# Kernel optimization log

Measured on AMD Instinct MI355X. Metric: run time of the kernel, lower is better.

Reference implementation:

```python
import jax, jax.numpy as jnp
import numpy as np

# Config (matches init_kwargs): 32 heads * 64 head_dim = intermediate 2048 = 2*1024
H, P, HID, N, G, K, CS = 32, 64, 1024, 128, 1, 4, 256
INTER = H * P                      # intermediate_size = expand * hidden_size
CONV_DIM = INTER + 2 * G * N       # 2304
PROJ = INTER + CONV_DIM + H        # 4384 (d_mlp == 0)
EPS = 1e-5


def segsum(x):
    """Stable segment sum: out[..., i, j] = sum_{j < k <= i} x[..., k]; -inf above diagonal."""
    T = x.shape[-1]
    xx = jnp.broadcast_to(x[..., None], x.shape + (T,))
    xx = jnp.where(jnp.tril(jnp.ones((T, T), bool), -1), xx, 0.0)
    s = jnp.cumsum(xx, axis=-2)
    return jnp.where(jnp.tril(jnp.ones((T, T), bool)), s, -jnp.inf)


def setup_inputs() -> dict:
    key = jax.random.key(0)
    ks = jax.random.split(key, 8)
    B_, S = 2, 2048
    x = jax.random.normal(ks[0], (B_, S, HID), jnp.float32)
    W_in = jax.random.normal(ks[1], (PROJ, HID), jnp.float32) / np.sqrt(HID)
    b_in = jnp.zeros((PROJ,), jnp.float32)
    conv_w = jax.random.normal(ks[2], (CONV_DIM, K), jnp.float32) / np.sqrt(K)
    # dt_bias = inverse-softplus of dt ~ LogUniform(1e-3, 0.1), as in __init__
    dt = jnp.exp(jax.random.uniform(ks[3], (H,)) * (np.log(0.1) - np.log(1e-3)) + np.log(1e-3))
    dt = jnp.clip(dt, 1e-4)
    dt_bias = dt + jnp.log(-jnp.expm1(-dt))
    A_log = jnp.log(jax.random.uniform(ks[4], (H,), minval=1.0, maxval=16.0))
    D = jnp.ones((H,), jnp.float32)
    norm_w = jnp.ones((INTER,), jnp.float32)
    W_out = jax.random.normal(ks[5], (HID, INTER), jnp.float32) / np.sqrt(INTER)
    b_out = jnp.zeros((HID,), jnp.float32)
    return {"x": x, "W_in": W_in, "b_in": b_in, "conv_w": conv_w, "dt_bias": dt_bias,
            "A_log": A_log, "D": D, "norm_w": norm_w, "W_out": W_out, "b_out": b_out}


def reference(x, W_in, b_in, conv_w, dt_bias, A_log, D, norm_w, W_out, b_out):
    B_, S, _ = x.shape
    proj = x @ W_in.T + b_in                               # (B,S,PROJ); d_mlp = 0
    gate = proj[..., :INTER]
    hBC = proj[..., INTER:INTER + CONV_DIM]
    dt = proj[..., INTER + CONV_DIM:]                      # (B,S,H)

    # depthwise causal conv1d (padding K-1, truncate to S) + silu
    xp = jnp.pad(hBC, ((0, 0), (K - 1, 0), (0, 0)))
    conv = sum(xp[:, i:i + S, :] * conv_w[:, i] for i in range(K))
    hBC = jax.nn.silu(conv)
    h = hBC[..., :INTER]
    Bm = hBC[..., INTER:INTER + G * N]
    Cm = hBC[..., INTER + G * N:]

    A = -jnp.exp(A_log.astype(jnp.float32))                # (H,)
    dt = jax.nn.softplus(dt + dt_bias)                     # (B,S,H); time_step_limit=(0,inf)
    h = h.reshape(B_, S, H, P).astype(jnp.float32)
    Bm = jnp.tile(Bm.reshape(B_, S, G, N).astype(jnp.float32), (1, 1, H // G, 1))
    Cm = jnp.tile(Cm.reshape(B_, S, G, N).astype(jnp.float32), (1, 1, H // G, 1))

    pad = (-S) % CS
    D_res = D[..., None] * jnp.pad(h, ((0, 0), (0, pad), (0, 0), (0, 0)))
    h = h * dt[..., None]
    Adt = A * dt                                           # (B,S,H)

    def chunk(t):
        t = jnp.pad(t, [(0, 0), (0, pad)] + [(0, 0)] * (t.ndim - 2))
        return t.reshape(B_, -1, CS, *t.shape[2:])

    h_c, B_c, C_c = chunk(h), chunk(Bm), chunk(Cm)         # (B,C,L,H,{P|N})
    A_c = chunk(Adt).transpose(0, 3, 1, 2)                 # (B,H,C,L)
    A_cum = jnp.cumsum(A_c, axis=-1)

    # 1) intra-chunk (diagonal blocks)
    Lmat = jnp.exp(segsum(A_c))                            # (B,H,C,L,L)
    Gm = jnp.einsum('bclhn,bcshn->bclsh', C_c, B_c)
    M = Gm * Lmat.transpose(0, 2, 3, 4, 1)
    Y_diag = jnp.einsum('bclsh,bcshp->bclhp', M, h_c)

    # 2) per-chunk final states
    decay = jnp.exp(A_cum[..., -1:] - A_cum)               # (B,H,C,L)
    B_decay = B_c * decay.transpose(0, 2, 3, 1)[..., None]
    states = jnp.einsum('bclhn,bclhp->bchpn', B_decay, h_c)

    # 3) inter-chunk state recurrence
    states = jnp.concatenate([jnp.zeros_like(states[:, :1]), states], axis=1)
    dc = jnp.exp(segsum(jnp.pad(A_cum[..., -1], ((0, 0), (0, 0), (1, 0)))))  # (B,H,C+1,C+1)
    states = jnp.einsum('bhij,bjhpn->bihpn', dc, states)[:, :-1]             # (B,C,H,P,N)

    # 4) state -> output
    sdo = jnp.exp(A_cum).transpose(0, 2, 3, 1)             # (B,C,L,H)
    Y_off = jnp.einsum('bclhn,bchpn->bclhp', C_c, states) * sdo[..., None]

    y = (Y_diag + Y_off).reshape(B_, -1, H, P) + D_res
    y = y[:, :S].reshape(B_, S, INTER)

    # gated RMSNorm (norm_before_gate=False): gate first, then normalize
    g = y * jax.nn.silu(gate.astype(jnp.float32))
    g = g * jax.lax.rsqrt(jnp.mean(g * g, axis=-1, keepdims=True) + EPS) * norm_w
    return g.astype(x.dtype) @ W_out.T + b_out
```

## Files before the change

### kernel.cpp

```cpp
#include <hip/hip_runtime.h>
#include <math.h>

#define Hh     32
#define Pp     64
#define HIDc   1024
#define Nn     128
#define CSc    256
#define INTERc 2048
#define CONVDc 2304
#define PROJc  4384
#define Bb     2
#define Ss     2048
#define Tt     4096
#define NCc    8
#define PROJ_PAD 4480

typedef __attribute__((ext_vector_type(8))) short short8_t;
typedef __attribute__((ext_vector_type(4))) float f32x4;
typedef unsigned short ushort_t;

__device__ __forceinline__ ushort_t f2b_rtn(float f) {
  unsigned u = __float_as_uint(f);
  unsigned lsb = (u >> 16) & 1u;
  u += 0x7fffu + lsb;
  return (ushort_t)(u >> 16);
}
__device__ __forceinline__ float b2f(ushort_t u) {
  return __uint_as_float(((unsigned)u) << 16);
}

__global__ __launch_bounds__(256)
void f2b_kernel(const float* __restrict__ in, ushort_t* __restrict__ out, int n8) {
  const int i = blockIdx.x * 256 + threadIdx.x;
  if (i >= n8) return;
  const float4* ip = (const float4*)in;
  float4 a = ip[2 * i], b = ip[2 * i + 1];
  union { short8_t v; ushort_t h[8]; } u;
  u.h[0] = f2b_rtn(a.x); u.h[1] = f2b_rtn(a.y);
  u.h[2] = f2b_rtn(a.z); u.h[3] = f2b_rtn(a.w);
  u.h[4] = f2b_rtn(b.x); u.h[5] = f2b_rtn(b.y);
  u.h[6] = f2b_rtn(b.z); u.h[7] = f2b_rtn(b.w);
  ((short8_t*)out)[i] = u.v;
}

__global__ __launch_bounds__(256)
void gemm_bf16(const ushort_t* __restrict__ A, const ushort_t* __restrict__ B,
               const float* __restrict__ bias, float* __restrict__ C,
               int M, int Nr, int K) {
  __shared__ ushort_t As[128 * 32];
  __shared__ ushort_t Bs[128 * 32];
  const int tid = threadIdx.x;
  const int lane = tid & 63, wid = tid >> 6;
  const int row0 = blockIdx.y * 128, col0 = blockIdx.x * 128;
  const int wr = (wid >> 1) * 64, wc = (wid & 1) * 64;
  const int fr = lane & 15;
  const int kq = (lane >> 4) * 8;

  f32x4 acc[4][4];
#pragma unroll
  for (int m = 0; m < 4; ++m)
#pragma unroll
    for (int n = 0; n < 4; ++n) acc[m][n] = (f32x4){0.f, 0.f, 0.f, 0.f};

  const int srow = (lane >> 2);
  const int skk = (lane & 3) * 8;

  for (int k0 = 0; k0 < K; k0 += 32) {
#pragma unroll
    for (int j = 0; j < 2; ++j) {
      const int s = wid * 2 + j;
      const int r = s * 16 + srow;
      const ushort_t* ga = A + (size_t)(row0 + r) * K + k0 + skk;
      const ushort_t* gb = B + (size_t)(col0 + r) * K + k0 + skk;
      __builtin_amdgcn_global_load_lds(
          (const __attribute__((address_space(1))) unsigned int*)ga,
          (__attribute__((address_space(3))) unsigned int*)(As + s * 512), 16, 0, 0);
      __builtin_amdgcn_global_load_lds(
          (const __attribute__((address_space(1))) unsigned int*)gb,
          (__attribute__((address_space(3))) unsigned int*)(Bs + s * 512), 16, 0, 0);
    }
    __syncthreads();
    short8_t av[4], bv[4];
#pragma unroll
    for (int m = 0; m < 4; ++m)
      av[m] = *(const short8_t*)(As + (wr + m * 16 + fr) * 32 + kq);
#pragma unroll
    for (int n = 0; n < 4; ++n)
      bv[n] = *(const short8_t*)(Bs + (wc + n * 16 + fr) * 32 + kq);
#pragma unroll
    for (int m = 0; m < 4; ++m)
#pragma unroll
      for (int n = 0; n < 4; ++n)
        acc[m][n] = __builtin_amdgcn_mfma_f32_16x16x32_bf16(av[m], bv[n],
                                                            acc[m][n], 0, 0, 0);
    __syncthreads();
  }

#pragma unroll
  for (int m = 0; m < 4; ++m) {
    const int r = row0 + wr + m * 16 + (lane >> 4) * 4;
#pragma unroll
    for (int n = 0; n < 4; ++n) {
      const int col = col0 + wc + n * 16 + fr;
      if (col < Nr) {
        const float bv_ = bias[col];
#pragma unroll
        for (int j = 0; j < 4; ++j)
          C[(size_t)(r + j) * Nr + col] = acc[m][n][j] + bv_;
      }
    }
  }
}

__global__ __launch_bounds__(256)
void conv_silu(const float* __restrict__ proj, const float* __restrict__ cw,
               float* __restrict__ conv) {
  const int idx = blockIdx.x * 256 + threadIdx.x;
  if (idx >= Tt * CONVDc) return;
  const int ch = idx % CONVDc;
  const int t  = idx / CONVDc;
  const int s  = t & (Ss - 1);
  const float4 w = *(const float4*)&cw[ch << 2];
  const float* col = proj + (size_t)t * PROJc + INTERc + ch;
  float acc;
  if (s >= 3) {
    acc = col[-(ptrdiff_t)3*PROJc]*w.x + col[-(ptrdiff_t)2*PROJc]*w.y
        + col[-(ptrdiff_t)PROJc]*w.z + col[0]*w.w;
  } else {
    acc = col[0]*w.w;
    if (s >= 1) acc += col[-(ptrdiff_t)PROJc]*w.z;
    if (s >= 2) acc += col[-(ptrdiff_t)2*PROJc]*w.y;
  }
  conv[idx] = acc / (1.f + __expf(-acc));
}

__global__ __launch_bounds__(256)
void dt_kernel(const float* __restrict__ proj, const float* __restrict__ dt_bias,
               const float* __restrict__ A_log, float* __restrict__ dtv,
               float* __restrict__ adt) {
  const int idx = blockIdx.x * 256 + threadIdx.x;
  const int hh = idx & (Hh - 1);
  const int t  = idx >> 5;
  float xv = proj[(size_t)t * PROJc + INTERc + CONVDc + hh] + dt_bias[hh];
  float sp = (xv > 20.f) ? xv : log1pf(__expf(xv));
  dtv[idx] = sp;
  adt[idx] = -__expf(A_log[hh]) * sp;
}

__global__ __launch_bounds__(256)
void scan_kernel(const float* __restrict__ adt, const float* __restrict__ dtv,
                 float* __restrict__ acumb, float* __restrict__ dtc) {
  const int g = blockIdx.x;
  const int h  = g & (Hh - 1);
  const int bc = g >> 5;
  const int b = bc >> 3, c = bc & 7;
  const int tid = threadIdx.x;
  const int lane = tid & 63, wv = tid >> 6;
  __shared__ float wsum[4];
  const int tg = b * Ss + c * CSc;
  float v  = adt[(size_t)(tg + tid) * Hh + h];
  float dv = dtv[(size_t)(tg + tid) * Hh + h];
#pragma unroll
  for (int off = 1; off < 64; off <<= 1) {
    float u = __shfl_up(v, off);
    if (lane >= off) v += u;
  }
  if (lane == 63) wsum[wv] = v;
  __syncthreads();
  float offacc = 0.f;
  for (int w = 0; w < wv; ++w) offacc += wsum[w];
  acumb[(size_t)g * CSc + tid] = v + offacc;
  dtc[(size_t)g * CSc + tid] = dv;
}

__global__ __launch_bounds__(256)
void bc_transpose(const float* __restrict__ conv, float* __restrict__ Bt,
                  float* __restrict__ Ct) {
  const int idx = blockIdx.x * 256 + threadIdx.x;
  const int s = idx & (Ss - 1);
  const int n = (idx >> 11) & (Nn - 1);
  const int b = idx >> 18;
  const size_t src = (size_t)(b * Ss + s) * CONVDc + INTERc;
  Bt[idx] = conv[src + n];
  Ct[idx] = conv[src + Nn + n];
}

__global__ __launch_bounds__(256)
void g_kernel(const float* __restrict__ Bt, const float* __restrict__ Ct,
              float* __restrict__ Gt) {
  const int bc = blockIdx.z;
  const int b = bc >> 3;
  const int c = bc & 7;
  const int l = blockIdx.y * 64 + (threadIdx.x & 63);
  const int s = blockIdx.x * 4 + (threadIdx.x >> 6);
  if (s > l) return;
  const int t0 = c * CSc;
  const float* cp = Ct + (size_t)b * Nn * Ss + t0 + l;
  const float* bp = Bt + (size_t)b * Nn * Ss + t0 + s;
  float acc = 0.f;
#pragma unroll 4
  for (int n = 0; n < Nn; ++n) acc += cp[(size_t)n * Ss] * bp[(size_t)n * Ss];
  Gt[((size_t)bc * CSc + s) * CSc + l] = acc;
}

#define ACC16(W, PTR)                                                          \
  {                                                                            \
    const float4* _p = (const float4*)(PTR);                                   \
    float4 _a = _p[0], _b = _p[1], _c = _p[2], _d = _p[3];                     \
    const float _w = (W);                                                      \
    acc[0] += _w*_a.x;  acc[1] += _w*_a.y;  acc[2] += _w*_a.z;  acc[3] += _w*_a.w; \
    acc[4] += _w*_b.x;  acc[5] += _w*_b.y;  acc[6] += _w*_b.z;  acc[7] += _w*_b.w; \
    acc[8] += _w*_c.x;  acc[9] += _w*_c.y;  acc[10]+= _w*_c.z;  acc[11]+= _w*_c.w; \
    acc[12]+= _w*_d.x;  acc[13]+= _w*_d.y;  acc[14]+= _w*_d.z;  acc[15]+= _w*_d.w; \
  }

__global__ __launch_bounds__(256)
void ssd_intra(const float* __restrict__ conv, const float* __restrict__ acumb,
               const float* __restrict__ dtc, const float* __restrict__ Gt,
               const float* __restrict__ Bt, const float* __restrict__ Dp,
               float* __restrict__ Y, float* __restrict__ S) {
  const int blk = blockIdx.x;
  const int h  = blk & 31;
  const int c  = (blk >> 5) & 7;
  const int b  = blk >> 8;
  const int bc = b * NCc + c;
  const int tg = b * Ss + c * CSc;
  const int tid = threadIdx.x;
  const int lane = tid & 63, wid = tid >> 6;
  const int fr = lane & 15, kq = lane >> 4;

  __shared__ ushort_t hrF[16384];
  __shared__ float acs[CSc];
  __shared__ float dts[CSc];
  __shared__ float wdec[CSc];

  {
    const size_t base = (size_t)(bc * Hh + h) * CSc;
    acs[tid] = acumb[base + tid];
    dts[tid] = dtc[base + tid];
  }
  __syncthreads();
  const float atot = acs[CSc - 1];
  wdec[tid] = __expf(atot - acs[tid]) * dts[tid];

  for (int i = tid; i < CSc * Pp; i += 256) {
    const int l = i >> 6, p = i & 63;
    float v = conv[(size_t)(tg + l) * CONVDc + h * Pp + p];
    const int off = ((l >> 5) * 4 + (p >> 4)) * 512 +
                    ((p & 15) + ((l >> 3) & 3) * 16) * 8 + (l & 7);
    hrF[off] = f2b_rtn(v);
  }
  __syncthreads();

  const int L0 = wid * 64;
  float al[4];
#pragma unroll
  for (int m = 0; m < 4; ++m) al[m] = acs[L0 + m * 16 + fr];

  f32x4 accY[4][4];
#pragma unroll
  for (int m = 0; m < 4; ++m)
#pragma unroll
    for (int n = 0; n < 4; ++n) accY[m][n] = (f32x4){0.f, 0.f, 0.f, 0.f};

  const float* gbase = Gt + (size_t)bc * CSc * CSc;
  const int kslim = 2 * wid + 2;
  for (int ks = 0; ks < kslim; ++ks) {
    short8_t bv[4];
#pragma unroll
    for (int pb = 0; pb < 4; ++pb)
      bv[pb] = *(const short8_t*)(hrF + ((ks * 4 + pb) * 64 + lane) * 8);
    const int sb2 = ks * 32 + kq * 8;
    short8_t av[4];
#pragma unroll
    for (int m = 0; m < 4; ++m) {
      const int l = L0 + m * 16 + fr;
      const float alm = al[m];
      union { short8_t v; ushort_t u[8]; } pk;
#pragma unroll
      for (int j = 0; j < 8; ++j) {
        const int s = sb2 + j;
        float g = gbase[(size_t)s * CSc + l];
        float w = g * __expf(alm - acs[s]) * dts[s];
        w = (s <= l) ? w : 0.f;
        pk.u[j] = f2b_rtn(w);
      }
      av[m] = pk.v;
    }
#pragma unroll
    for (int m = 0; m < 4; ++m)
#pragma unroll
      for (int pb = 0; pb < 4; ++pb)
        accY[m][pb] = __builtin_amdgcn_mfma_f32_16x16x32_bf16(av[m], bv[pb],
                                                              accY[m][pb], 0, 0, 0);
  }

  const float Dh = Dp[h];
#pragma unroll
  for (int m = 0; m < 4; ++m) {
#pragma unroll
    for (int pb = 0; pb < 4; ++pb) {
      const int p = pb * 16 + fr;
#pragma unroll
      for (int j = 0; j < 4; ++j) {
        const int l = L0 + m * 16 + kq * 4 + j;
        const int off = ((l >> 5) * 4 + pb) * 512 +
                        (fr + ((l >> 3) & 3) * 16) * 8 + (l & 7);
        Y[(size_t)(tg + l) * INTERc + h * Pp + p] =
            accY[m][pb][j] + Dh * b2f(hrF[off]);
      }
    }
  }

  f32x4 accS[4][2];
#pragma unroll
  for (int m = 0; m < 4; ++m)
#pragma unroll
    for (int n = 0; n < 2; ++n) accS[m][n] = (f32x4){0.f, 0.f, 0.f, 0.f};

  const int N0 = wid * 32;
  const float* btb = Bt + (size_t)b * Nn * Ss + c * CSc;
  for (int ks = 0; ks < 8; ++ks) {
    short8_t am[4];
#pragma unroll
    for (int m = 0; m < 4; ++m)
      am[m] = *(const short8_t*)(hrF + ((ks * 4 + m) * 64 + lane) * 8);
    const int l0 = ks * 32 + kq * 8;
    short8_t bn[2];
#pragma unroll
    for (int nf = 0; nf < 2; ++nf) {
      const int n = N0 + nf * 16 + fr;
      const float* bp = btb + (size_t)n * Ss + l0;
      float4 v0 = *(const float4*)bp;
      float4 v1 = *(const float4*)(bp + 4);
      union { short8_t v; ushort_t u[8]; } pk;
      pk.u[0] = f2b_rtn(v0.x * wdec[l0 + 0]);
      pk.u[1] = f2b_rtn(v0.y * wdec[l0 + 1]);
      pk.u[2] = f2b_rtn(v0.z * wdec[l0 + 2]);
      pk.u[3] = f2b_rtn(v0.w * wdec[l0 + 3]);
      pk.u[4] = f2b_rtn(v1.x * wdec[l0 + 4]);
      pk.u[5] = f2b_rtn(v1.y * wdec[l0 + 5]);
      pk.u[6] = f2b_rtn(v1.z * wdec[l0 + 6]);
      pk.u[7] = f2b_rtn(v1.w * wdec[l0 + 7]);
      bn[nf] = pk.v;
    }
#pragma unroll
    for (int m = 0; m < 4; ++m)
#pragma unroll
      for (int nf = 0; nf < 2; ++nf)
        accS[m][nf] = __builtin_amdgcn_mfma_f32_16x16x32_bf16(am[m], bn[nf],
                                                              accS[m][nf], 0, 0, 0);
  }

  float* sp = S + ((size_t)bc * Hh + h) * Pp * Nn;
#pragma unroll
  for (int m = 0; m < 4; ++m)
#pragma unroll
    for (int nf = 0; nf < 2; ++nf) {
      const int n = N0 + nf * 16 + fr;
#pragma unroll
      for (int j = 0; j < 4; ++j)
        sp[(size_t)(m * 16 + kq * 4 + j) * Nn + n] = accS[m][nf][j];
    }
}

__global__ __launch_bounds__(256)
void state_combine(const float* __restrict__ S, const float* __restrict__ acumb,
                   float* __restrict__ R) {
  const int idx = blockIdx.x * 256 + threadIdx.x;
  const int n = idx & 127;
  const int p = (idx >> 7) & 63;
  const int h = (idx >> 13) & 31;
  const int b = idx >> 18;
  float r = 0.f;
  for (int c = 0; c < NCc; ++c) {
    const int bc = b * NCc + c;
    const size_t off = (((size_t)bc * Hh + h) * Pp + p) * Nn + n;
    R[off] = r;
    const float atot = acumb[((size_t)bc * Hh + h) * CSc + CSc - 1];
    r = r * __expf(atot) + S[off];
  }
}

__global__ __launch_bounds__(256)
void ssd_off(const float* __restrict__ Ct, const float* __restrict__ acumb,
             const float* __restrict__ R, float* __restrict__ Y) {
  const int blk = blockIdx.x;
  const int pb = blk & 3;
  const int h  = (blk >> 2) & 31;
  const int c  = (blk >> 7) & 7;
  const int b  = blk >> 10;
  const int p0 = pb * 16;
  const int bc = b * NCc + c;
  const int tg = b * Ss + c * CSc;
  const int tid = threadIdx.x;

  __shared__ float stateT[Nn][20];
  {
    const size_t rbase = (((size_t)bc * Hh + h) * Pp + p0) * Nn;
    for (int i = tid; i < Nn * 16; i += 256) {
      const int pp = i >> 7, n = i & 127;
      stateT[n][pp] = R[rbase + (size_t)pp * Nn + n];
    }
  }
  __syncthreads();
  const int l = tid;
  const float el = __expf(acumb[((size_t)bc * Hh + h) * CSc + l]);
  float acc[16];
#pragma unroll
  for (int q = 0; q < 16; ++q) acc[q] = 0.f;
  const float* cp = Ct + (size_t)b * Nn * Ss + c * CSc + l;
#pragma unroll 4
  for (int n = 0; n < Nn; ++n) {
    float cv = cp[(size_t)n * Ss];
    ACC16(cv, &stateT[n][0]);
  }
  float* yp = Y + (size_t)(tg + l) * INTERc + h * Pp + p0;
  float4 y0 = ((float4*)yp)[0], y1 = ((float4*)yp)[1];
  float4 y2 = ((float4*)yp)[2], y3 = ((float4*)yp)[3];
  ((float4*)yp)[0] = make_float4(y0.x + el*acc[0],  y0.y + el*acc[1],  y0.z + el*acc[2],  y0.w + el*acc[3]);
  ((float4*)yp)[1] = make_float4(y1.x + el*acc[4],  y1.y + el*acc[5],  y1.z + el*acc[6],  y1.w + el*acc[7]);
  ((float4*)yp)[2] = make_float4(y2.x + el*acc[8],  y2.y + el*acc[9],  y2.z + el*acc[10], y2.w + el*acc[11]);
  ((float4*)yp)[3] = make_float4(y3.x + el*acc[12], y3.y + el*acc[13], y3.z + el*acc[14], y3.w + el*acc[15]);
}

__global__ __launch_bounds__(256)
void gate_norm(const float* __restrict__ Y, const float* __restrict__ proj,
               const float* __restrict__ nw, ushort_t* __restrict__ g) {
  const int t = blockIdx.x;
  const int tid = threadIdx.x;
  const int lane = tid & 63, wv = tid >> 6;
  __shared__ float ws4[4];
  const float* yp = Y + (size_t)t * INTERc;
  const float* gp = proj + (size_t)t * PROJc;
  float vals[8];
  float ss = 0.f;
#pragma unroll
  for (int i = 0; i < 8; ++i) {
    const int cix = tid + (i << 8);
    float yv = yp[cix];
    float gv = gp[cix];
    float vv = yv * (gv / (1.f + __expf(-gv)));
    vals[i] = vv;
    ss += vv * vv;
  }
#pragma unroll
  for (int off = 32; off > 0; off >>= 1) ss += __shfl_xor(ss, off);
  if (lane == 0) ws4[wv] = ss;
  __syncthreads();
  const float tot = ws4[0] + ws4[1] + ws4[2] + ws4[3];
  const float sc = rsqrtf(tot * (1.f / INTERc) + 1e-5f);
  ushort_t* go = g + (size_t)t * INTERc;
#pragma unroll
  for (int i = 0; i < 8; ++i) {
    const int cix = tid + (i << 8);
    go[cix] = f2b_rtn(vals[i] * sc * nw[cix]);
  }
}

extern "C" void kernel_launch(void* const* d_in, const int* in_sizes, int n_in,
                              void* d_out, int out_size, void* d_ws, size_t ws_size,
                              hipStream_t stream) {
  (void)in_sizes; (void)n_in; (void)out_size; (void)ws_size;
  const float* x       = (const float*)d_in[0];
  const float* W_in    = (const float*)d_in[1];
  const float* b_in    = (const float*)d_in[2];
  const float* conv_w  = (const float*)d_in[3];
  const float* dt_bias = (const float*)d_in[4];
  const float* A_log   = (const float*)d_in[5];
  const float* Dp      = (const float*)d_in[6];
  const float* norm_w  = (const float*)d_in[7];
  const float* W_out   = (const float*)d_in[8];
  const float* b_out   = (const float*)d_in[9];
  float* out = (float*)d_out;

  float* proj  = (float*)d_ws;
  float* conv  = proj  + (size_t)Tt * PROJc;
  float* dtv   = conv  + (size_t)Tt * CONVDc;
  float* adt   = dtv   + (size_t)Tt * Hh;
  float* Bt    = adt   + (size_t)Tt * Hh;
  float* Ct    = Bt    + (size_t)Bb * Nn * Ss;
  float* Gt    = Ct    + (size_t)Bb * Nn * Ss;
  float* acumb = Gt    + (size_t)Bb * NCc * CSc * CSc;
  float* dtc   = acumb + (size_t)Bb * NCc * Hh * CSc;
  float* Sbuf  = dtc   + (size_t)Bb * NCc * Hh * CSc;
  float* Roff  = Sbuf  + (size_t)Bb * NCc * Hh * Pp * Nn;
  float* Ybuf  = Roff  + (size_t)Bb * NCc * Hh * Pp * Nn;

  ushort_t* xb  = (ushort_t*)Sbuf;
  ushort_t* Wib = (ushort_t*)Roff;
  ushort_t* Wob = (ushort_t*)Gt;
  ushort_t* gbb = (ushort_t*)conv;

  f2b_kernel<<<(Tt * HIDc / 8 + 255) / 256, 256, 0, stream>>>(x, xb, Tt * HIDc / 8);
  f2b_kernel<<<(PROJc * HIDc / 8 + 255) / 256, 256, 0, stream>>>(
      W_in, Wib, PROJc * HIDc / 8);
  gemm_bf16<<<dim3(PROJ_PAD / 128, Tt / 128), 256, 0, stream>>>(
      xb, Wib, b_in, proj, Tt, PROJc, HIDc);
  conv_silu<<<(Tt * CONVDc) / 256, 256, 0, stream>>>(proj, conv_w, conv);
  dt_kernel<<<(Tt * Hh) / 256, 256, 0, stream>>>(proj, dt_bias, A_log, dtv, adt);
  scan_kernel<<<Bb * NCc * Hh, 256, 0, stream>>>(adt, dtv, acumb, dtc);
  bc_transpose<<<(Bb * Nn * Ss) / 256, 256, 0, stream>>>(conv, Bt, Ct);
  g_kernel<<<dim3(64, 4, 16), 256, 0, stream>>>(Bt, Ct, Gt);
  ssd_intra<<<Bb * NCc * Hh, 256, 0, stream>>>(conv, acumb, dtc, Gt, Bt, Dp,
                                               Ybuf, Sbuf);
  state_combine<<<(Bb * Hh * Pp * Nn) / 256, 256, 0, stream>>>(Sbuf, acumb, Roff);
  ssd_off<<<Bb * NCc * Hh * 4, 256, 0, stream>>>(Ct, acumb, Roff, Ybuf);
  f2b_kernel<<<(HIDc * INTERc / 8 + 255) / 256, 256, 0, stream>>>(
      W_out, Wob, HIDc * INTERc / 8);
  gate_norm<<<Tt, 256, 0, stream>>>(Ybuf, proj, norm_w, gbb);
  gemm_bf16<<<dim3(HIDc / 128, Tt / 128), 256, 0, stream>>>(
      gbb, Wob, b_out, out, Tt, HIDc, INTERc);
}
```

Baseline: 399.4 us.

## Add 256x256 double-buffered GEMM with LDS swizzle and XCD-aware block mapping

```diff
diff --git a/kernel.cpp b/kernel.cpp
--- a/kernel.cpp
+++ b/kernel.cpp
@@ -13,7 +13,7 @@
 #define Ss     2048
 #define Tt     4096
 #define NCc    8
-#define PROJ_PAD 4480
+#define PROJ_PAD 4608
 
 typedef __attribute__((ext_vector_type(8))) short short8_t;
 typedef __attribute__((ext_vector_type(4))) float f32x4;
@@ -27,6 +27,12 @@
 }
 __device__ __forceinline__ float b2f(ushort_t u) {
   return __uint_as_float(((unsigned)u) << 16);
+}
+
+__device__ __forceinline__ int xcd_swz(int bid, int nwg) {
+  const int q = nwg >> 3, r = nwg & 7;
+  const int xcd = bid & 7, loc = bid >> 3;
+  return (xcd < r ? xcd * (q + 1) : r * (q + 1) + (xcd - r) * q) + loc;
 }
 
 __global__ __launch_bounds__(256)
@@ -43,18 +49,114 @@
   ((short8_t*)out)[i] = u.v;
 }
 
+__global__ __launch_bounds__(512, 2)
+void gemm256(const ushort_t* __restrict__ A, const ushort_t* __restrict__ B,
+             const float* __restrict__ bias, float* __restrict__ C,
+             int M, int Nr, int K, int nbx) {
+  __shared__ ushort_t lds[2][2][256 * 64];
+  int bid = xcd_swz(blockIdx.x, gridDim.x);
+  const int bx = bid % nbx, by = bid / nbx;
+  const int row0 = by * 256, col0 = bx * 256;
+  const int tid = threadIdx.x;
+  const int lane = tid & 63, wid = tid >> 6;
+  const int wm = wid >> 2, wn = wid & 3;
+  const int fr = lane & 15, kq = lane >> 4;
+
+  const int srow = lane >> 3;
+  const int sq = (lane & 7) ^ ((lane >> 3) & 7);
+  const int KT = K >> 6;
+
+  f32x4 acc[8][4];
+#pragma unroll
+  for (int m = 0; m < 8; ++m)
+#pragma unroll
+    for (int n = 0; n < 4; ++n) acc[m][n] = (f32x4){0.f, 0.f, 0.f, 0.f};
+
+  auto stage = [&](int buf, int kt) {
+    const int k0 = kt << 6;
+#pragma unroll
+    for (int i = 0; i < 4; ++i) {
+      const int g = wid * 4 + i;
+      const int r = g * 8 + srow;
+      const ushort_t* ga = A + (size_t)(row0 + r) * K + k0 + sq * 8;
+      const ushort_t* gb = B + (size_t)(col0 + r) * K + k0 + sq * 8;
+      __builtin_amdgcn_global_load_lds(
+          (const __attribute__((address_space(1))) unsigned int*)ga,
+          (__attribute__((address_space(3))) unsigned int*)(&lds[buf][0][0] + g * 512),
+          16, 0, 0);
+      __builtin_amdgcn_global_load_lds(
+          (const __attribute__((address_space(1))) unsigned int*)gb,
+          (__attribute__((address_space(3))) unsigned int*)(&lds[buf][1][0] + g * 512),
+          16, 0, 0);
+    }
+  };
+
+  stage(0, 0);
+  __syncthreads();
+  int cur = 0;
+  for (int kt = 0; kt < KT; ++kt) {
+    if (kt + 1 < KT) stage(cur ^ 1, kt + 1);
+    const ushort_t* As = &lds[cur][0][0];
+    const ushort_t* Bs = &lds[cur][1][0];
+    __builtin_amdgcn_s_setprio(1);
+#pragma unroll
+    for (int ksub = 0; ksub < 2; ++ksub) {
+      const int q = ksub * 4 + kq;
+      short8_t av[8], bv[4];
+#pragma unroll
+      for (int m = 0; m < 8; ++m) {
+        const int r = wm * 128 + m * 16 + fr;
+        av[m] = *(const short8_t*)(As + r * 64 + (q ^ (r & 7)) * 8);
+      }
+#pragma unroll
+      for (int n = 0; n < 4; ++n) {
+        const int r = wn * 64 + n * 16 + fr;
+        bv[n] = *(const short8_t*)(Bs + r * 64 + (q ^ (r & 7)) * 8);
+      }
+#pragma unroll
+      for (int m = 0; m < 8; ++m)
+#pragma unroll
+        for (int n = 0; n < 4; ++n)
+          acc[m][n] = __builtin_amdgcn_mfma_f32_16x16x32_bf16(av[m], bv[n],
+                                                              acc[m][n], 0, 0, 0);
+    }
+    __builtin_amdgcn_s_setprio(0);
+    __syncthreads();
+    cur ^= 1;
+  }
+
+#pragma unroll
+  for (int m = 0; m < 8; ++m) {
+    const int r = row0 + wm * 128 + m * 16 + kq * 4;
+#pragma unroll
+    for (int n = 0; n < 4; ++n) {
+      const int col = col0 + wn * 64 + n * 16 + fr;
+      if (col < Nr) {
+        const float bv_ = bias[col];
+#pragma unroll
+        for (int j = 0; j < 4; ++j)
+          C[(size_t)(r + j) * Nr + col] = acc[m][n][j] + bv_;
+      }
+    }
+  }
+}
+
 __global__ __launch_bounds__(256)
 void gemm_bf16(const ushort_t* __restrict__ A, const ushort_t* __restrict__ B,
                const float* __restrict__ bias, float* __restrict__ C,
-               int M, int Nr, int K) {
-  __shared__ ushort_t As[128 * 32];
-  __shared__ ushort_t Bs[128 * 32];
+               int M, int Nr, int K, int nbx) {
+  __shared__ ushort_t lds[2][2][128 * 32];
+  int bid = xcd_swz(blockIdx.x, gridDim.x);
+  const int bx = bid % nbx, by = bid / nbx;
+  const int row0 = by * 128, col0 = bx * 128;
   const int tid = threadIdx.x;
   const int lane = tid & 63, wid = tid >> 6;
-  const int row0 = blockIdx.y * 128, col0 = blockIdx.x * 128;
   const int wr = (wid >> 1) * 64, wc = (wid & 1) * 64;
-  const int fr = lane & 15;
-  const int kq = (lane >> 4) * 8;
+  const int fr = lane & 15, kq = lane >> 4;
+
+  const int srow = lane >> 2;
+  const int sq = ((lane & 3) - ((lane >> 3) & 3)) & 3;
+  const int KT = K >> 5;
 
   f32x4 acc[4][4];
 #pragma unroll
@@ -62,31 +164,43 @@
 #pragma unroll
     for (int n = 0; n < 4; ++n) acc[m][n] = (f32x4){0.f, 0.f, 0.f, 0.f};
 
-  const int srow = (lane >> 2);
-  const int skk = (lane & 3) * 8;
-
-  for (int k0 = 0; k0 < K; k0 += 32) {
+  auto stage = [&](int buf, int kt) {
+    const int k0 = kt << 5;
 #pragma unroll
     for (int j = 0; j < 2; ++j) {
-      const int s = wid * 2 + j;
-      const int r = s * 16 + srow;
-      const ushort_t* ga = A + (size_t)(row0 + r) * K + k0 + skk;
-      const ushort_t* gb = B + (size_t)(col0 + r) * K + k0 + skk;
+      const int g = wid * 2 + j;
+      const int r = g * 16 + srow;
+      const ushort_t* ga = A + (size_t)(row0 + r) * K + k0 + sq * 8;
+      const ushort_t* gb = B + (size_t)(col0 + r) * K + k0 + sq * 8;
       __builtin_amdgcn_global_load_lds(
           (const __attribute__((address_space(1))) unsigned int*)ga,
-          (__attribute__((address_space(3))) unsigned int*)(As + s * 512), 16, 0, 0);
+          (__attribute__((address_space(3))) unsigned int*)(&lds[buf][0][0] + g * 512),
+          16, 0, 0);
       __builtin_amdgcn_global_load_lds(
           (const __attribute__((address_space(1))) unsigned int*)gb,
-          (__attribute__((address_space(3))) unsigned int*)(Bs + s * 512), 16, 0, 0);
-    }
-    __syncthreads();
+          (__attribute__((address_space(3))) unsigned int*)(&lds[buf][1][0] + g * 512),
+          16, 0, 0);
+    }
+  };
+
+  stage(0, 0);
+  __syncthreads();
+  int cur = 0;
+  for (int kt = 0; kt < KT; ++kt) {
+    if (kt + 1 < KT) stage(cur ^ 1, kt + 1);
+    const ushort_t* As = &lds[cur][0][0];
+    const ushort_t* Bs = &lds[cur][1][0];
     short8_t av[4], bv[4];
 #pragma unroll
-    for (int m = 0; m < 4; ++m)
-      av[m] = *(const short8_t*)(As + (wr + m * 16 + fr) * 32 + kq);
-#pragma unroll
-    for (int n = 0; n < 4; ++n)
-      bv[n] = *(const short8_t*)(Bs + (wc + n * 16 + fr) * 32 + kq);
+    for (int m = 0; m < 4; ++m) {
+      const int r = wr + m * 16 + fr;
+      av[m] = *(const short8_t*)(As + r * 32 + ((kq + ((r >> 1) & 3)) & 3) * 8);
+    }
+#pragma unroll
+    for (int n = 0; n < 4; ++n) {
+      const int r = wc + n * 16 + fr;
+      bv[n] = *(const short8_t*)(Bs + r * 32 + ((kq + ((r >> 1) & 3)) & 3) * 8);
+    }
 #pragma unroll
     for (int m = 0; m < 4; ++m)
 #pragma unroll
@@ -94,11 +208,12 @@
         acc[m][n] = __builtin_amdgcn_mfma_f32_16x16x32_bf16(av[m], bv[n],
                                                             acc[m][n], 0, 0, 0);
     __syncthreads();
+    cur ^= 1;
   }
 
 #pragma unroll
   for (int m = 0; m < 4; ++m) {
-    const int r = row0 + wr + m * 16 + (lane >> 4) * 4;
+    const int r = row0 + wr + m * 16 + kq * 4;
 #pragma unroll
     for (int n = 0; n < 4; ++n) {
       const int col = col0 + wc + n * 16 + fr;
@@ -495,8 +610,8 @@
   f2b_kernel<<<(Tt * HIDc / 8 + 255) / 256, 256, 0, stream>>>(x, xb, Tt * HIDc / 8);
   f2b_kernel<<<(PROJc * HIDc / 8 + 255) / 256, 256, 0, stream>>>(
       W_in, Wib, PROJc * HIDc / 8);
-  gemm_bf16<<<dim3(PROJ_PAD / 128, Tt / 128), 256, 0, stream>>>(
-      xb, Wib, b_in, proj, Tt, PROJc, HIDc);
+  gemm256<<<(PROJ_PAD / 256) * (Tt / 256), 512, 0, stream>>>(
+      xb, Wib, b_in, proj, Tt, PROJc, HIDc, PROJ_PAD / 256);
   conv_silu<<<(Tt * CONVDc) / 256, 256, 0, stream>>>(proj, conv_w, conv);
   dt_kernel<<<(Tt * Hh) / 256, 256, 0, stream>>>(proj, dt_bias, A_log, dtv, adt);
   scan_kernel<<<Bb * NCc * Hh, 256, 0, stream>>>(adt, dtv, acumb, dtc);
@@ -509,6 +624,6 @@
   f2b_kernel<<<(HIDc * INTERc / 8 + 255) / 256, 256, 0, stream>>>(
       W_out, Wob, HIDc * INTERc / 8);
   gate_norm<<<Tt, 256, 0, stream>>>(Ybuf, proj, norm_w, gbb);
-  gemm_bf16<<<dim3(HIDc / 128, Tt / 128), 256, 0, stream>>>(
-      gbb, Wob, b_out, out, Tt, HIDc, INTERc);
-}
+  gemm_bf16<<<(HIDc / 128) * (Tt / 128), 256, 0, stream>>>(
+      gbb, Wob, b_out, out, Tt, HIDc, INTERc, HIDc / 128);
+}
```

Result: faster. 382.5 us (-4.2%).
